# Kernel tuning notes

Measured on AMD Instinct MI355X. Metric: run time of the kernel, lower is better.

Reference implementation:

```python
import jax, jax.numpy as jnp
import numpy as np

QMIN, QMAX = -128, 127  # get_quantized_range(8)


def setup_inputs() -> dict:
    key = jax.random.key(0)
    k1, k2, k3, k4 = jax.random.split(key, 4)
    N, IN, OUT = 8192, 4096, 4096
    x = jax.random.randint(k1, (N, IN), QMIN, QMAX + 1, dtype=jnp.int32).astype(jnp.int8)
    weight = jax.random.randint(k2, (OUT, IN), QMIN, QMAX + 1, dtype=jnp.int32).astype(jnp.int8)
    bias = jax.random.randint(k3, (OUT,), -1000, 1000, dtype=jnp.int32)
    weight_scale = jax.random.uniform(k4, (OUT,), dtype=jnp.float32, minval=1e-3, maxval=2e-2)
    return {
        "x": x,
        "weight": weight,
        "bias": bias,
        "weight_scale": weight_scale,
        "input_scale": 0.05,
        "output_scale": 0.1,
        "output_zero_point": -3,
    }


def reference(x, weight, bias, weight_scale, input_scale, output_scale, output_zero_point):
    # int8 GEMM accumulated in int32 (matches CPU path of the torch code)
    acc = jnp.matmul(x.astype(jnp.int32), weight.astype(jnp.int32).T) + bias[None, :]
    # fused per-channel dequant/requant epilogue
    scale = (input_scale * weight_scale / output_scale)[None, :]  # [1, OUT]
    out = acc.astype(jnp.float32) * scale + output_zero_point
    out = jnp.clip(jnp.round(out), QMIN, QMAX).astype(jnp.int8)
    return out
```

## Files before the change

### kernel.cpp

```cpp
#include <hip/hip_runtime.h>
#include <stdint.h>
#include <stddef.h>

typedef int v4i __attribute__((ext_vector_type(4)));

#define GLOAD16(gp, lp) __builtin_amdgcn_global_load_lds( \
    (const __attribute__((address_space(1))) void*)(gp),  \
    (__attribute__((address_space(3))) void*)(lp), 16, 0, 0)

#define PH_BAR()     __builtin_amdgcn_s_barrier()
#define WAIT_VM(n)   asm volatile("s_waitcnt vmcnt(" #n ")" ::: "memory")
#define SCHED_FENCE() __builtin_amdgcn_sched_barrier(0)
#define PRIO1() __builtin_amdgcn_s_setprio(1)
#define PRIO0() __builtin_amdgcn_s_setprio(0)

static __device__ __forceinline__ int pack4(int a, int b, int c, int d) {
    return (a & 255) | ((b & 255) << 8) | ((c & 255) << 16) | (d << 24);
}

__global__ __launch_bounds__(256) void pack2_kernel(const int* __restrict__ srcA, v4i* __restrict__ dstA, int nA,
                                                    const int* __restrict__ srcB, v4i* __restrict__ dstB, int nB) {
    int i = blockIdx.x * blockDim.x + threadIdx.x;
    const int* src; v4i* dst;
    if (i < nA) { src = srcA; dst = dstA; }
    else { i -= nA; if (i >= nB) return; src = srcB; dst = dstB; }
    const v4i* s = reinterpret_cast<const v4i*>(src) + (size_t)i * 4;
    v4i v0 = s[0], v1 = s[1], v2 = s[2], v3 = s[3];
    v4i r;
    r.x = pack4(v0.x, v0.y, v0.z, v0.w);
    r.y = pack4(v1.x, v1.y, v1.z, v1.w);
    r.z = pack4(v2.x, v2.y, v2.z, v2.w);
    r.w = pack4(v3.x, v3.y, v3.z, v3.w);
    dst[i] = r;
}

__global__ __launch_bounds__(512, 1) void gemm_q8_8ph(
    const char* __restrict__ Apk, const char* __restrict__ Bpk,
    const int* __restrict__ bias, const float* __restrict__ wscale,
    const float* __restrict__ is_p, const float* __restrict__ os_p,
    const int* __restrict__ zp_p,
    int* __restrict__ out, int K, int Ncols)
{
    __shared__ char lds[98304];

    const int tid  = threadIdx.x;
    const int wid  = tid >> 6;
    const int lane = tid & 63;
    const int l7 = lane & 7, l3 = lane >> 3;
    const int lo16 = lane & 15, hi = lane >> 4;

    int swz;
    {
        const int nwg = gridDim.x;
        const int q = nwg >> 3, r = nwg & 7;
        const int xcd = blockIdx.x & 7;
        const int base = (xcd < r) ? xcd * (q + 1) : r * (q + 1) + (xcd - r) * q;
        swz = base + (blockIdx.x >> 3);
    }
    const int nbc  = Ncols >> 7;
    const int brow = swz / nbc, bcol = swz % nbc;

    const int wr = wid >> 1, wc = wid & 1;

    const char* Ab = Apk + (size_t)(brow * 256 + wid * 8 + l3) * K + ((l7 ^ l3) << 4);
    const char* Bb = Bpk + (size_t)(bcol * 128 + wid * 8 + l3) * K + ((l7 ^ l3) << 4);

    const int colsw0 = (hi ^ l7) << 4;
    const int colsw1 = colsw0 ^ 64;
    const int aBase = (wr << 13) + (lo16 << 7);
    const int bBase = 65536 + (wc << 13) + (lo16 << 7);

    v4i acc[4][4];
#pragma unroll
    for (int m = 0; m < 4; ++m)
#pragma unroll
        for (int n = 0; n < 4; ++n)
            acc[m][n] = (v4i){0, 0, 0, 0};

    v4i afA[2][2], afB[2][2], bfE[4][2], bfO[4][2];

    auto stageA = [&](int par, int h, int t) {
        const char* g = Ab + (size_t)(h * 128) * K + ((size_t)t << 7);
        char* l = lds + (par + (h << 14) + (wid << 10));
        GLOAD16(g, l);
        GLOAD16(g + (size_t)64 * K, l + 8192);
    };
    auto stageB = [&](int par, int t) {
        const char* g = Bb + ((size_t)t << 7);
        char* l = lds + (65536 + par + (wid << 10));
        GLOAD16(g, l);
        GLOAD16(g + (size_t)64 * K, l + 8192);
    };
    auto ldA = [&](v4i (&dst)[2][2], int par, int mh) {
#pragma unroll
        for (int m = 0; m < 2; ++m) {
            const int base = par + aBase + (mh << 12) + (m << 11);
            dst[m][0] = *(const v4i*)(lds + base + colsw0);
            dst[m][1] = *(const v4i*)(lds + base + colsw1);
        }
    };
    auto ldB2 = [&](v4i (&dst)[4][2], int par, int n0) {
#pragma unroll
        for (int k = 0; k < 2; ++k) {
            const int n = n0 + k;
            const int base = bBase + par + (n << 11);
            dst[n][0] = *(const v4i*)(lds + base + colsw0);
            dst[n][1] = *(const v4i*)(lds + base + colsw1);
        }
    };

#define MQ(afX, bfY, mo) do {                                                     \
    _Pragma("unroll") for (int m_ = 0; m_ < 2; ++m_)                              \
    _Pragma("unroll") for (int n_ = 0; n_ < 4; ++n_)                              \
    _Pragma("unroll") for (int s_ = 0; s_ < 2; ++s_)                              \
        acc[(mo) + m_][n_] = __builtin_amdgcn_mfma_i32_16x16x64_i8(               \
            afX[m_][s_], bfY[n_][s_], acc[(mo) + m_][n_], 0, 0, 0);               \
} while (0)

    stageA(0, 0, 0);      stageA(0, 1, 0);
    stageB(0, 0);
    stageB(16384, 1);
    stageA(32768, 0, 1);  stageA(32768, 1, 1);
    WAIT_VM(4);
    PH_BAR();
    SCHED_FENCE();
    ldA(afA, 0, 0);
    ldB2(bfE, 0, 0);  ldB2(bfE, 0, 2);

    const int niter = K >> 8;
    for (int i = 0; i < niter - 1; ++i) {
        const int tE2 = 2 * i + 2, tO2 = 2 * i + 3;

        SCHED_FENCE();
        ldA(afB, 0, 1);
        ldB2(bfO, 16384, 0);
        stageB(0, tE2);
        SCHED_FENCE();
        PRIO1(); MQ(afA, bfE, 0); PRIO0();
        WAIT_VM(2);
        PH_BAR();
        SCHED_FENCE();
        ldA(afA, 32768, 0);
        ldB2(bfO, 16384, 2);
        stageA(0, 0, tE2);  stageA(0, 1, tE2);
        SCHED_FENCE();
        PRIO1(); MQ(afB, bfE, 2); PRIO0();
        WAIT_VM(4);
        PH_BAR();
        SCHED_FENCE();
        ldA(afB, 32768, 1);
        ldB2(bfE, 0, 0);
        stageB(16384, tO2);
        SCHED_FENCE();
        PRIO1(); MQ(afA, bfO, 0); PRIO0();
        WAIT_VM(2);
        PH_BAR();
        SCHED_FENCE();
        ldA(afA, 0, 0);
        ldB2(bfE, 0, 2);
        stageA(32768, 0, tO2);  stageA(32768, 1, tO2);
        SCHED_FENCE();
        PRIO1(); MQ(afB, bfO, 2); PRIO0();
        WAIT_VM(4);
        PH_BAR();
    }

    {
        SCHED_FENCE();
        ldA(afB, 0, 1);
        ldB2(bfO, 16384, 0);
        SCHED_FENCE();
        PRIO1(); MQ(afA, bfE, 0); PRIO0();
        WAIT_VM(0);
        PH_BAR();
        SCHED_FENCE();
        ldA(afA, 32768, 0);
        ldB2(bfO, 16384, 2);
        SCHED_FENCE();
        PRIO1(); MQ(afB, bfE, 2); PRIO0();
        SCHED_FENCE();
        ldA(afB, 32768, 1);
        SCHED_FENCE();
        PRIO1(); MQ(afA, bfO, 0); PRIO0();
        PRIO1(); MQ(afB, bfO, 2); PRIO0();
    }
#undef MQ

    const float is = *is_p, os = *os_p;
    const float zp = (float)(*zp_p);
    const int colb = (bcol << 7) + (wc << 6) + lo16;
    float sc[4]; int bv[4];
#pragma unroll
    for (int n = 0; n < 4; ++n) {
        sc[n] = is * wscale[colb + (n << 4)] / os;
        bv[n] = bias[colb + (n << 4)];
    }
#pragma unroll
    for (int m = 0; m < 4; ++m) {
#pragma unroll
        for (int j = 0; j < 4; ++j) {
            const int row = (brow << 8) + (wr << 6) + (m << 4) + (hi << 2) + j;
            int* op = out + (size_t)row * Ncols + colb;
#pragma unroll
            for (int n = 0; n < 4; ++n) {
                float f = (float)(acc[m][n][j] + bv[n]) * sc[n] + zp;
                f = rintf(f);
                f = fminf(fmaxf(f, -128.f), 127.f);
                op[n << 4] = (int)f;
            }
        }
    }
}

template <bool PACKED>
__global__ __launch_bounds__(256) void gemm_q8(
    const void* __restrict__ Ain, const void* __restrict__ Bin,
    const int* __restrict__ bias, const float* __restrict__ wscale,
    const float* __restrict__ is_p, const float* __restrict__ os_p,
    const int* __restrict__ zp_p,
    int* __restrict__ out, int Nrows, int K, int Ncols)
{
    __shared__ char Al[128 * 64];
    __shared__ char Bl[128 * 64];

    const int tid  = threadIdx.x;
    const int wid  = tid >> 6;
    const int lane = tid & 63;

    const int nbc = Ncols / 128;
    int swz = blockIdx.x;
    if ((gridDim.x & 7) == 0) {
        const int cpx = gridDim.x >> 3;
        swz = (blockIdx.x & 7) * cpx + (blockIdx.x >> 3);
    }
    const int brow = swz / nbc;
    const int bcol = swz % nbc;
    const int wr = wid >> 1, wc = wid & 1;

    v4i acc[4][4];
#pragma unroll
    for (int m = 0; m < 4; ++m)
#pragma unroll
        for (int n = 0; n < 4; ++n)
            acc[m][n] = (v4i){0, 0, 0, 0};

    const char* Ag = nullptr;
    const char* Bg = nullptr;
    if (PACKED) {
        Ag = (const char*)Ain + (size_t)(brow * 128 + wid * 32 + (lane >> 2)) * K + (lane & 3) * 16;
        Bg = (const char*)Bin + (size_t)(bcol * 128 + wid * 32 + (lane >> 2)) * K + (lane & 3) * 16;
    }
    char* aldst = Al + wid * 2048;
    char* bldst = Bl + wid * 2048;

    const int lo16 = lane & 15, hi = lane >> 4;
    const int aoff0 = (wr * 64 + lo16) * 64 + hi * 16;
    const int boff0 = (wc * 64 + lo16) * 64 + hi * 16;

    for (int k0 = 0; k0 < K; k0 += 64) {
        if (PACKED) {
            GLOAD16(Ag + k0,          aldst);
            GLOAD16(Ag + 16 * K + k0, aldst + 1024);
            GLOAD16(Bg + k0,          bldst);
            GLOAD16(Bg + 16 * K + k0, bldst + 1024);
        } else {
            const int row = tid >> 1, half = tid & 1;
            const int* sA = (const int*)Ain + (size_t)(brow * 128 + row) * K + k0 + half * 32;
            const int* sB = (const int*)Bin + (size_t)(bcol * 128 + row) * K + k0 + half * 32;
            int pa[8], pb[8];
#pragma unroll
            for (int j = 0; j < 8; ++j) {
                v4i va = reinterpret_cast<const v4i*>(sA)[j];
                v4i vb = reinterpret_cast<const v4i*>(sB)[j];
                pa[j] = pack4(va.x, va.y, va.z, va.w);
                pb[j] = pack4(vb.x, vb.y, vb.z, vb.w);
            }
            v4i* da = (v4i*)&Al[row * 64 + half * 32];
            da[0] = (v4i){pa[0], pa[1], pa[2], pa[3]};
            da[1] = (v4i){pa[4], pa[5], pa[6], pa[7]};
            v4i* db = (v4i*)&Bl[row * 64 + half * 32];
            db[0] = (v4i){pb[0], pb[1], pb[2], pb[3]};
            db[1] = (v4i){pb[4], pb[5], pb[6], pb[7]};
        }
        __syncthreads();

        v4i afr[4], bfr[4];
#pragma unroll
        for (int m = 0; m < 4; ++m)
            afr[m] = *(const v4i*)&Al[aoff0 + m * 16 * 64];
#pragma unroll
        for (int n = 0; n < 4; ++n)
            bfr[n] = *(const v4i*)&Bl[boff0 + n * 16 * 64];
#pragma unroll
        for (int m = 0; m < 4; ++m)
#pragma unroll
            for (int n = 0; n < 4; ++n)
                acc[m][n] = __builtin_amdgcn_mfma_i32_16x16x64_i8(afr[m], bfr[n], acc[m][n], 0, 0, 0);

        __syncthreads();
    }

    const float is = *is_p;
    const float os = *os_p;
    const float zp = (float)(*zp_p);
#pragma unroll
    for (int n = 0; n < 4; ++n) {
        const int col = bcol * 128 + wc * 64 + n * 16 + lo16;
        const float sc = is * wscale[col] / os;
        const int   bv = bias[col];
#pragma unroll
        for (int m = 0; m < 4; ++m) {
            const int row0 = brow * 128 + wr * 64 + m * 16 + hi * 4;
#pragma unroll
            for (int j = 0; j < 4; ++j) {
                float f = (float)(acc[m][n][j] + bv) * sc + zp;
                f = rintf(f);
                f = fminf(fmaxf(f, -128.f), 127.f);
                out[(size_t)(row0 + j) * Ncols + col] = (int)f;
            }
        }
    }
}

extern "C" void kernel_launch(void* const* d_in, const int* in_sizes, int n_in,
                              void* d_out, int out_size, void* d_ws, size_t ws_size,
                              hipStream_t stream) {
    const int*   x32    = (const int*)d_in[0];
    const int*   w32    = (const int*)d_in[1];
    const int*   bias   = (const int*)d_in[2];
    const float* wscale = (const float*)d_in[3];
    const float* isp    = (const float*)d_in[4];
    const float* osp    = (const float*)d_in[5];
    const int*   zpp    = (const int*)d_in[6];
    int* out = (int*)d_out;

    const int OUT = in_sizes[2];
    const int K   = in_sizes[1] / OUT;
    const int Nr  = in_sizes[0] / K;

    const size_t need = (size_t)Nr * K + (size_t)OUT * K;

    if (ws_size >= need) {
        char* xpk = (char*)d_ws;
        char* wpk = xpk + (size_t)Nr * K;
        const int nx16 = (Nr * K) / 16;
        const int nw16 = (OUT * K) / 16;
        pack2_kernel<<<(nx16 + nw16 + 255) / 256, 256, 0, stream>>>(
            x32, (v4i*)xpk, nx16, w32, (v4i*)wpk, nw16);
        if ((Nr & 255) == 0 && (OUT & 127) == 0 && (K & 255) == 0 && (K >> 8) >= 2) {
            const int grid8 = (Nr / 256) * (OUT / 128);
            gemm_q8_8ph<<<grid8, 512, 0, stream>>>(xpk, wpk, bias, wscale, isp, osp, zpp,
                                                   out, K, OUT);
        } else {
            const int grid = (Nr / 128) * (OUT / 128);
            gemm_q8<true><<<grid, 256, 0, stream>>>(xpk, wpk, bias, wscale, isp, osp, zpp,
                                                    out, Nr, K, OUT);
        }
    } else {
        const int grid = (Nr / 128) * (OUT / 128);
        gemm_q8<false><<<grid, 256, 0, stream>>>(x32, w32, bias, wscale, isp, osp, zpp,
                                                 out, Nr, K, OUT);
    }
}
```

Baseline: 191.2 us.

## Enlarge GEMM block tile to 256x256 with double-buffered K=128 stages

The int8 GEMM main kernel now computes 256x256 output tiles per 512-thread block instead of 256x128. Each wave owns 128x64 (8x4 MFMA tiles). The pipeline becomes a simple two-buffer scheme over K-steps of 128 using 128KB of LDS, and each B fragment is loaded once and reused across four A fragment pairs. This is meant to raise arithmetic intensity and cut global/LDS traffic per MFMA. The cost is more accumulator registers (128 VGPRs for acc), fewer blocks in the grid (512 for this shape), full LDS use, and a wait for all outstanding loads each iteration.

```diff
diff --git a/kernel.cpp b/kernel.cpp
--- a/kernel.cpp
+++ b/kernel.cpp
@@ -34,14 +34,14 @@
     dst[i] = r;
 }
 
-__global__ __launch_bounds__(512, 1) void gemm_q8_8ph(
+__global__ __launch_bounds__(512, 1) void gemm_q8_mp(
     const char* __restrict__ Apk, const char* __restrict__ Bpk,
     const int* __restrict__ bias, const float* __restrict__ wscale,
     const float* __restrict__ is_p, const float* __restrict__ os_p,
     const int* __restrict__ zp_p,
     int* __restrict__ out, int K, int Ncols)
 {
-    __shared__ char lds[98304];
+    __shared__ char lds[131072];
 
     const int tid  = threadIdx.x;
     const int wid  = tid >> 6;
@@ -57,138 +57,122 @@
         const int base = (xcd < r) ? xcd * (q + 1) : r * (q + 1) + (xcd - r) * q;
         swz = base + (blockIdx.x >> 3);
     }
-    const int nbc  = Ncols >> 7;
+    const int nbc  = Ncols >> 8;
     const int brow = swz / nbc, bcol = swz % nbc;
 
-    const int wr = wid >> 1, wc = wid & 1;
+    const int wr = wid >> 2, wc = wid & 3;
 
     const char* Ab = Apk + (size_t)(brow * 256 + wid * 8 + l3) * K + ((l7 ^ l3) << 4);
-    const char* Bb = Bpk + (size_t)(bcol * 128 + wid * 8 + l3) * K + ((l7 ^ l3) << 4);
+    const char* Bb = Bpk + (size_t)(bcol * 256 + wid * 8 + l3) * K + ((l7 ^ l3) << 4);
 
     const int colsw0 = (hi ^ l7) << 4;
     const int colsw1 = colsw0 ^ 64;
-    const int aBase = (wr << 13) + (lo16 << 7);
-    const int bBase = 65536 + (wc << 13) + (lo16 << 7);
-
-    v4i acc[4][4];
-#pragma unroll
-    for (int m = 0; m < 4; ++m)
+    const int aBase = (wr << 14) + (lo16 << 7);
+    const int bBase = (wc << 13) + (lo16 << 7);
+
+    v4i acc[8][4];
+#pragma unroll
+    for (int m = 0; m < 8; ++m)
 #pragma unroll
         for (int n = 0; n < 4; ++n)
             acc[m][n] = (v4i){0, 0, 0, 0};
 
-    v4i afA[2][2], afB[2][2], bfE[4][2], bfO[4][2];
-
-    auto stageA = [&](int par, int h, int t) {
-        const char* g = Ab + (size_t)(h * 128) * K + ((size_t)t << 7);
-        char* l = lds + (par + (h << 14) + (wid << 10));
+    v4i afA[2][2], afB[2][2], bf[4][2];
+
+    auto stage = [&](const char* gb, int ldsOff, int h, int t) {
+        const char* g = gb + (size_t)(h * 128) * K + ((size_t)t << 7);
+        char* l = lds + (ldsOff + (h << 14) + (wid << 10));
         GLOAD16(g, l);
         GLOAD16(g + (size_t)64 * K, l + 8192);
     };
-    auto stageB = [&](int par, int t) {
-        const char* g = Bb + ((size_t)t << 7);
-        char* l = lds + (65536 + par + (wid << 10));
-        GLOAD16(g, l);
-        GLOAD16(g + (size_t)64 * K, l + 8192);
-    };
-    auto ldA = [&](v4i (&dst)[2][2], int par, int mh) {
+    auto ldAf = [&](v4i (&dst)[2][2], int bufo, int pair) {
 #pragma unroll
         for (int m = 0; m < 2; ++m) {
-            const int base = par + aBase + (mh << 12) + (m << 11);
+            const int base = bufo + aBase + (pair << 12) + (m << 11);
             dst[m][0] = *(const v4i*)(lds + base + colsw0);
             dst[m][1] = *(const v4i*)(lds + base + colsw1);
         }
     };
-    auto ldB2 = [&](v4i (&dst)[4][2], int par, int n0) {
-#pragma unroll
-        for (int k = 0; k < 2; ++k) {
-            const int n = n0 + k;
-            const int base = bBase + par + (n << 11);
-            dst[n][0] = *(const v4i*)(lds + base + colsw0);
-            dst[n][1] = *(const v4i*)(lds + base + colsw1);
-        }
+    auto ldBf = [&](int bufo) {
+#pragma unroll
+        for (int n = 0; n < 4; ++n)
+            bf[n][0] = *(const v4i*)(lds + 65536 + bufo + bBase + (n << 11) + colsw0);
+#pragma unroll
+        for (int n = 0; n < 4; ++n)
+            bf[n][1] = *(const v4i*)(lds + 65536 + bufo + bBase + (n << 11) + colsw1);
     };
 
-#define MQ(afX, bfY, mo) do {                                                     \
+#define MQ(afX, p) do {                                                           \
+    _Pragma("unroll") for (int s_ = 0; s_ < 2; ++s_)                              \
     _Pragma("unroll") for (int m_ = 0; m_ < 2; ++m_)                              \
     _Pragma("unroll") for (int n_ = 0; n_ < 4; ++n_)                              \
-    _Pragma("unroll") for (int s_ = 0; s_ < 2; ++s_)                              \
-        acc[(mo) + m_][n_] = __builtin_amdgcn_mfma_i32_16x16x64_i8(               \
-            afX[m_][s_], bfY[n_][s_], acc[(mo) + m_][n_], 0, 0, 0);               \
+        acc[((p) << 1) + m_][n_] = __builtin_amdgcn_mfma_i32_16x16x64_i8(         \
+            afX[m_][s_], bf[n_][s_], acc[((p) << 1) + m_][n_], 0, 0, 0);          \
 } while (0)
 
-    stageA(0, 0, 0);      stageA(0, 1, 0);
-    stageB(0, 0);
-    stageB(16384, 1);
-    stageA(32768, 0, 1);  stageA(32768, 1, 1);
-    WAIT_VM(4);
+    stage(Ab, 0,     0, 0);  stage(Ab, 0,     1, 0);
+    stage(Bb, 65536, 0, 0);  stage(Bb, 65536, 1, 0);
+    WAIT_VM(0);
     PH_BAR();
     SCHED_FENCE();
-    ldA(afA, 0, 0);
-    ldB2(bfE, 0, 0);  ldB2(bfE, 0, 2);
-
-    const int niter = K >> 8;
-    for (int i = 0; i < niter - 1; ++i) {
-        const int tE2 = 2 * i + 2, tO2 = 2 * i + 3;
-
-        SCHED_FENCE();
-        ldA(afB, 0, 1);
-        ldB2(bfO, 16384, 0);
-        stageB(0, tE2);
-        SCHED_FENCE();
-        PRIO1(); MQ(afA, bfE, 0); PRIO0();
-        WAIT_VM(2);
-        PH_BAR();
-        SCHED_FENCE();
-        ldA(afA, 32768, 0);
-        ldB2(bfO, 16384, 2);
-        stageA(0, 0, tE2);  stageA(0, 1, tE2);
-        SCHED_FENCE();
-        PRIO1(); MQ(afB, bfE, 2); PRIO0();
-        WAIT_VM(4);
-        PH_BAR();
-        SCHED_FENCE();
-        ldA(afB, 32768, 1);
-        ldB2(bfE, 0, 0);
-        stageB(16384, tO2);
-        SCHED_FENCE();
-        PRIO1(); MQ(afA, bfO, 0); PRIO0();
-        WAIT_VM(2);
-        PH_BAR();
-        SCHED_FENCE();
-        ldA(afA, 0, 0);
-        ldB2(bfE, 0, 2);
-        stageA(32768, 0, tO2);  stageA(32768, 1, tO2);
-        SCHED_FENCE();
-        PRIO1(); MQ(afB, bfO, 2); PRIO0();
-        WAIT_VM(4);
+    ldAf(afA, 0, 0);
+
+    const int nt = K >> 7;
+    for (int t = 0; t < nt - 1; ++t) {
+        const int b  = (t & 1) << 15;
+        const int nb = (~t & 1) << 15;
+
+        SCHED_FENCE();
+        ldBf(b);
+        ldAf(afB, b, 1);
+        stage(Ab, nb, 0, t + 1);  stage(Ab, nb, 1, t + 1);
+        SCHED_FENCE();
+        PRIO1(); MQ(afA, 0); PRIO0();
+        PH_BAR();
+        SCHED_FENCE();
+        ldAf(afA, b, 2);
+        stage(Bb, 65536 + nb, 0, t + 1);  stage(Bb, 65536 + nb, 1, t + 1);
+        SCHED_FENCE();
+        PRIO1(); MQ(afB, 1); PRIO0();
+        PH_BAR();
+        SCHED_FENCE();
+        ldAf(afB, b, 3);
+        SCHED_FENCE();
+        PRIO1(); MQ(afA, 2); PRIO0();
+        WAIT_VM(0);
+        PH_BAR();
+        SCHED_FENCE();
+        ldAf(afA, nb, 0);
+        SCHED_FENCE();
+        PRIO1(); MQ(afB, 3); PRIO0();
         PH_BAR();
     }
 
     {
-        SCHED_FENCE();
-        ldA(afB, 0, 1);
-        ldB2(bfO, 16384, 0);
-        SCHED_FENCE();
-        PRIO1(); MQ(afA, bfE, 0); PRIO0();
-        WAIT_VM(0);
-        PH_BAR();
-        SCHED_FENCE();
-        ldA(afA, 32768, 0);
-        ldB2(bfO, 16384, 2);
-        SCHED_FENCE();
-        PRIO1(); MQ(afB, bfE, 2); PRIO0();
-        SCHED_FENCE();
-        ldA(afB, 32768, 1);
-        SCHED_FENCE();
-        PRIO1(); MQ(afA, bfO, 0); PRIO0();
-        PRIO1(); MQ(afB, bfO, 2); PRIO0();
+        const int b = ((nt - 1) & 1) << 15;
+        SCHED_FENCE();
+        ldBf(b);
+        ldAf(afB, b, 1);
+        SCHED_FENCE();
+        PRIO1(); MQ(afA, 0); PRIO0();
+        PH_BAR();
+        SCHED_FENCE();
+        ldAf(afA, b, 2);
+        SCHED_FENCE();
+        PRIO1(); MQ(afB, 1); PRIO0();
+        PH_BAR();
+        SCHED_FENCE();
+        ldAf(afB, b, 3);
+        SCHED_FENCE();
+        PRIO1(); MQ(afA, 2); PRIO0();
+        PH_BAR();
+        PRIO1(); MQ(afB, 3); PRIO0();
     }
 #undef MQ
 
     const float is = *is_p, os = *os_p;
     const float zp = (float)(*zp_p);
-    const int colb = (bcol << 7) + (wc << 6) + lo16;
+    const int colb = (bcol << 8) + (wc << 6) + lo16;
     float sc[4]; int bv[4];
 #pragma unroll
     for (int n = 0; n < 4; ++n) {
@@ -196,10 +180,10 @@
         bv[n] = bias[colb + (n << 4)];
     }
 #pragma unroll
-    for (int m = 0; m < 4; ++m) {
+    for (int m = 0; m < 8; ++m) {
 #pragma unroll
         for (int j = 0; j < 4; ++j) {
-            const int row = (brow << 8) + (wr << 6) + (m << 4) + (hi << 2) + j;
+            const int row = (brow << 8) + (wr << 7) + (m << 4) + (hi << 2) + j;
             int* op = out + (size_t)row * Ncols + colb;
 #pragma unroll
             for (int n = 0; n < 4; ++n) {
@@ -347,10 +331,10 @@
         const int nw16 = (OUT * K) / 16;
         pack2_kernel<<<(nx16 + nw16 + 255) / 256, 256, 0, stream>>>(
             x32, (v4i*)xpk, nx16, w32, (v4i*)wpk, nw16);
-        if ((Nr & 255) == 0 && (OUT & 127) == 0 && (K & 255) == 0 && (K >> 8) >= 2) {
-            const int grid8 = (Nr / 256) * (OUT / 128);
-            gemm_q8_8ph<<<grid8, 512, 0, stream>>>(xpk, wpk, bias, wscale, isp, osp, zpp,
-                                                   out, K, OUT);
+        if ((Nr & 255) == 0 && (OUT & 255) == 0 && (K & 127) == 0 && (K >> 7) >= 2) {
+            const int grid8 = (Nr / 256) * (OUT / 256);
+            gemm_q8_mp<<<grid8, 512, 0, stream>>>(xpk, wpk, bias, wscale, isp, osp, zpp,
+                                                  out, K, OUT);
         } else {
             const int grid = (Nr / 128) * (OUT / 128);
             gemm_q8<true><<<grid, 256, 0, stream>>>(xpk, wpk, bias, wscale, isp, osp, zpp,
```

Result: faster. 177.4 us (-7.2%).
